# Kernel tuning notes

Hardware: AMD Instinct MI355X
Metric: run time of the kernel (lower is better)

Reference implementation:

```python
import jax, jax.numpy as jnp
import numpy as np

DT = 0.002   # solver step used for drive indexing
B = 2097152  # batched independent circuits (trailing axis of y)
T = 50000    # external drive time steps
NP = 59      # number of clamped scalar parameters


def setup_inputs() -> dict:
    key = jax.random.key(0)
    k1, k2, k3 = jax.random.split(key, 3)
    params = jax.random.uniform(k1, (NP,), jnp.float32, 0.5, 10.0)
    bounds_lo = jnp.full((NP,), 0.01, dtype=jnp.float32)
    bounds_hi = jnp.full((NP,), 100.0, dtype=jnp.float32)
    t = jnp.float32(12.345)
    y = jax.random.normal(k2, (12, B), jnp.float32) * 5.0
    external_drive = jax.random.normal(k3, (T, 6), jnp.float32)
    return {"params": params, "bounds_lo": bounds_lo, "bounds_hi": bounds_hi,
            "t": t, "y": y, "external_drive": external_drive}


def _S(v, e0, v0, r):
    # sigmoidal firing-rate function
    return 2.0 * e0 / (1.0 + jnp.exp(r * (v0 - v)))


def reference(params, bounds_lo, bounds_hi, t, y, external_drive):
    p = jnp.clip(params, bounds_lo, bounds_hi)
    (A_p23_p23, A_p23_p5, A_p23_st, A_p23_PV, A_p23_SST, A_p23_VIP, a_p23, e0_p23, v0_p23, r_p23,
     A_p5_p5, A_p5_st, A_p5_PV, A_p5_SST, a_p5, e0_p5, v0_p5, r_p5,
     A_st_p23, A_st_p5, A_st_st, A_st_PV, A_st_SST, a_st, e0_st, v0_st, r_st,
     B_PV_p23, B_PV_p5, B_PV_st, B_PV_PV, B_PV_SST, B_PV_VIP, b_PV, e0_PV, v0_PV, r_PV,
     B_SST_p23, B_SST_p5, B_SST_PV, B_SST_SST, B_SST_VIP, b_SST, e0_SST, v0_SST, r_SST,
     B_VIP_PV, B_VIP_SST, B_VIP_VIP, b_VIP, e0_VIP, v0_VIP, r_VIP,
     N_p23, N_p5, N_st, N_PV, N_SST, N_VIP) = p

    P23, P5, St, PV, SST, VIP, dP23, dP5, dSt, dPV, dSST, dVIP = y  # each [B]

    F_P23 = _S(P23, e0_p23, v0_p23, r_p23)
    F_P5  = _S(P5,  e0_p5,  v0_p5,  r_p5)
    F_St  = _S(St,  e0_st,  v0_st,  r_st)
    F_PV  = _S(PV,  e0_PV,  v0_PV,  r_PV)
    F_SST = _S(SST, e0_SST, v0_SST, r_SST)
    F_VIP = _S(VIP, e0_VIP, v0_VIP, r_VIP)

    n_t = external_drive.shape[0]
    t_idx = jnp.clip(t / DT, 0.0, n_t - 1).astype(jnp.int32)
    drive = jax.lax.dynamic_index_in_dim(external_drive, t_idx, axis=0, keepdims=False)  # [6]
    cc_p23, th_p5, th_st, th_PV, nm_SST, cc_VIP = drive[0], drive[1], drive[2], drive[3], drive[4], drive[5]

    dy6 = (cc_p23 + A_st_p23 * a_st * F_St * (N_st / N_p23)
           + A_p23_p23 * a_p23 * F_P23
           - B_PV_p23 * b_PV * F_PV * (N_PV / N_p23)
           - B_SST_p23 * b_SST * F_SST * (N_SST / N_p23)
           - 2.0 * a_p23 * dP23 - a_p23 ** 2 * P23)
    dy7 = (th_p5 + A_st_p5 * a_st * F_St * (N_st / N_p5)
           + A_p23_p5 * a_p23 * F_P23 * (N_p23 / N_p5)
           + A_p5_p5 * a_p5 * F_P5
           - B_PV_p5 * b_PV * F_PV * (N_PV / N_p5)
           - B_SST_p5 * b_SST * F_SST * (N_SST / N_p5)
           - 2.0 * a_p5 * dP5 - a_p5 ** 2 * P5)
    dy8 = (th_st + A_p23_st * a_p23 * F_P23 * (N_p23 / N_st)
           + A_p5_st * a_p5 * F_P5 * (N_p5 / N_st)
           - B_PV_st * b_PV * F_PV * (N_PV / N_st)
           - 2.0 * a_st * dSt - a_st ** 2 * St)
    dy9 = (th_PV + A_p23_PV * a_p23 * F_P23 * (N_p23 / N_PV)
           + A_p5_PV * a_p5 * F_P5 * (N_p5 / N_PV)
           + A_st_PV * a_st * F_St * (N_st / N_PV)
           - B_PV_PV * b_PV * F_PV
           - B_SST_PV * b_SST * F_SST * (N_SST / N_PV)
           - B_VIP_PV * b_VIP * F_VIP * (N_VIP / N_PV)
           - 2.0 * b_PV * dPV - b_PV ** 2 * PV)
    dy10 = (nm_SST + A_p23_SST * a_p23 * F_P23 * (N_p23 / N_SST)
            + A_p5_SST * a_p5 * F_P5 * (N_p5 / N_SST)
            + A_st_SST * a_st * F_St * (N_st / N_SST)
            - B_PV_SST * b_PV * F_PV * (N_PV / N_SST)
            - B_SST_SST * b_SST * F_SST
            - B_VIP_SST * b_VIP * F_VIP * (N_VIP / N_SST)
            - 2.0 * b_SST * dSST - b_SST ** 2 * SST)
    dy11 = (cc_VIP + A_p23_VIP * a_p23 * F_P23 * (N_p23 / N_VIP)
            - B_PV_VIP * b_PV * F_PV * (N_PV / N_VIP)
            - B_SST_VIP * b_SST * F_SST * (N_SST / N_VIP)
            - B_VIP_VIP * b_VIP * F_VIP
            - 2.0 * b_VIP * dVIP - b_VIP ** 2 * VIP)

    return jnp.stack([dP23, dP5, dSt, dPV, dSST, dVIP, dy6, dy7, dy8, dy9, dy10, dy11])
```

## Files before the change

kernel.cpp:

```cpp
#include <hip/hip_runtime.h>
#include <math.h>


__global__ __launch_bounds__(256) void cc_kernel(
    const float* __restrict__ params,
    const float* __restrict__ blo,
    const float* __restrict__ bhi,
    const float* __restrict__ tptr,
    const float* __restrict__ y,
    const float* __restrict__ drive,
    float* __restrict__ out,
    int n, int tsteps)
{
    __shared__ float sc[72];
    __shared__ float p[59];

    const int tid = threadIdx.x;
    if (tid < 59) {
        float v = params[tid];
        p[tid] = fminf(fmaxf(v, blo[tid]), bhi[tid]);
    }
    __syncthreads();

    if (tid == 0) {
        float A_p23_p23=p[0], A_p23_p5=p[1], A_p23_st=p[2], A_p23_PV=p[3],
              A_p23_SST=p[4], A_p23_VIP=p[5], a_p23=p[6], e0_p23=p[7],
              v0_p23=p[8], r_p23=p[9];
        float A_p5_p5=p[10], A_p5_st=p[11], A_p5_PV=p[12], A_p5_SST=p[13],
              a_p5=p[14], e0_p5=p[15], v0_p5=p[16], r_p5=p[17];
        float A_st_p23=p[18], A_st_p5=p[19], A_st_PV=p[21],
              A_st_SST=p[22], a_st=p[23], e0_st=p[24], v0_st=p[25], r_st=p[26];
        float B_PV_p23=p[27], B_PV_p5=p[28], B_PV_st=p[29], B_PV_PV=p[30],
              B_PV_SST=p[31], B_PV_VIP=p[32], b_PV=p[33], e0_PV=p[34],
              v0_PV=p[35], r_PV=p[36];
        float B_SST_p23=p[37], B_SST_p5=p[38], B_SST_PV=p[39], B_SST_SST=p[40],
              B_SST_VIP=p[41], b_SST=p[42], e0_SST=p[43], v0_SST=p[44], r_SST=p[45];
        float B_VIP_PV=p[46], B_VIP_SST=p[47], B_VIP_VIP=p[48], b_VIP=p[49],
              e0_VIP=p[50], v0_VIP=p[51], r_VIP=p[52];
        float N_p23=p[53], N_p5=p[54], N_st=p[55], N_PV=p[56], N_SST=p[57], N_VIP=p[58];

        const float rr[6] = {r_p23, r_p5, r_st, r_PV, r_SST, r_VIP};
        const float vv[6] = {v0_p23, v0_p5, v0_st, v0_PV, v0_SST, v0_VIP};
        const float ee[6] = {e0_p23, e0_p5, e0_st, e0_PV, e0_SST, e0_VIP};
        const float gg[6] = {a_p23, a_p5, a_st, b_PV, b_SST, b_VIP};
        for (int k = 0; k < 6; ++k) {
            sc[k]      = rr[k];
            sc[6 + k]  = rr[k] * vv[k];
            sc[12 + k] = 2.0f * ee[k];
            sc[18 + k] = 2.0f * gg[k];
            sc[24 + k] = gg[k] * gg[k];
        }

        float t = *tptr;
        float fi = fminf(fmaxf(t / 0.002f, 0.0f), (float)(tsteps - 1));
        int ti = (int)fi;
        for (int k = 0; k < 6; ++k) sc[30 + k] = drive[(size_t)ti * 6 + k];

        float M[36];
        for (int i = 0; i < 36; ++i) M[i] = 0.0f;
        M[0*6+0] =  A_p23_p23 * a_p23;
        M[0*6+2] =  A_st_p23  * a_st  * (N_st  / N_p23);
        M[0*6+3] = -B_PV_p23  * b_PV  * (N_PV  / N_p23);
        M[0*6+4] = -B_SST_p23 * b_SST * (N_SST / N_p23);

        M[1*6+0] =  A_p23_p5  * a_p23 * (N_p23 / N_p5);
        M[1*6+1] =  A_p5_p5   * a_p5;
        M[1*6+2] =  A_st_p5   * a_st  * (N_st  / N_p5);
        M[1*6+3] = -B_PV_p5   * b_PV  * (N_PV  / N_p5);
        M[1*6+4] = -B_SST_p5  * b_SST * (N_SST / N_p5);

        M[2*6+0] =  A_p23_st  * a_p23 * (N_p23 / N_st);
        M[2*6+1] =  A_p5_st   * a_p5  * (N_p5  / N_st);
        M[2*6+3] = -B_PV_st   * b_PV  * (N_PV  / N_st);

        M[3*6+0] =  A_p23_PV  * a_p23 * (N_p23 / N_PV);
        M[3*6+1] =  A_p5_PV   * a_p5  * (N_p5  / N_PV);
        M[3*6+2] =  A_st_PV   * a_st  * (N_st  / N_PV);
        M[3*6+3] = -B_PV_PV   * b_PV;
        M[3*6+4] = -B_SST_PV  * b_SST * (N_SST / N_PV);
        M[3*6+5] = -B_VIP_PV  * b_VIP * (N_VIP / N_PV);

        M[4*6+0] =  A_p23_SST * a_p23 * (N_p23 / N_SST);
        M[4*6+1] =  A_p5_SST  * a_p5  * (N_p5  / N_SST);
        M[4*6+2] =  A_st_SST  * a_st  * (N_st  / N_SST);
        M[4*6+3] = -B_PV_SST  * b_PV  * (N_PV  / N_SST);
        M[4*6+4] = -B_SST_SST * b_SST;
        M[4*6+5] = -B_VIP_SST * b_VIP * (N_VIP / N_SST);

        M[5*6+0] =  A_p23_VIP * a_p23 * (N_p23 / N_VIP);
        M[5*6+3] = -B_PV_VIP  * b_PV  * (N_PV  / N_VIP);
        M[5*6+4] = -B_SST_VIP * b_SST * (N_SST / N_VIP);
        M[5*6+5] = -B_VIP_VIP * b_VIP;

        for (int i = 0; i < 36; ++i) sc[36 + i] = M[i];
    }
    __syncthreads();

    const size_t i4 = ((size_t)blockIdx.x * blockDim.x + threadIdx.x) * 4;
    if (i4 + 3 >= (size_t)n && i4 >= (size_t)n) return;

    float4 v[12];
#pragma unroll
    for (int r = 0; r < 12; ++r)
        v[r] = *(const float4*)(y + (size_t)r * n + i4);

#pragma unroll
    for (int r = 0; r < 6; ++r)
        *(float4*)(out + (size_t)r * n + i4) = v[6 + r];

    float F[6][4];
#pragma unroll
    for (int k = 0; k < 6; ++k) {
        const float rk  = sc[k];
        const float rv0 = sc[6 + k];
        const float e2  = sc[12 + k];
        const float* vk = (const float*)&v[k];
#pragma unroll
        for (int j = 0; j < 4; ++j)
            F[k][j] = e2 / (1.0f + __expf(rv0 - rk * vk[j]));
    }

#pragma unroll
    for (int i = 0; i < 6; ++i) {
        const float dr  = sc[30 + i];
        const float tg  = sc[18 + i];
        const float gsq = sc[24 + i];
        const float* vi = (const float*)&v[i];
        const float* di = (const float*)&v[6 + i];
        float4 o;
        float* op = (float*)&o;
#pragma unroll
        for (int j = 0; j < 4; ++j) {
            float acc = dr;
#pragma unroll
            for (int k = 0; k < 6; ++k)
                acc = fmaf(sc[36 + i * 6 + k], F[k][j], acc);
            acc = fmaf(-tg, di[j], acc);
            acc = fmaf(-gsq, vi[j], acc);
            op[j] = acc;
        }
        *(float4*)(out + (size_t)(6 + i) * n + i4) = o;
    }
}

extern "C" void kernel_launch(void* const* d_in, const int* in_sizes, int n_in,
                              void* d_out, int out_size, void* d_ws, size_t ws_size,
                              hipStream_t stream) {
    const float* params = (const float*)d_in[0];
    const float* blo    = (const float*)d_in[1];
    const float* bhi    = (const float*)d_in[2];
    const float* tptr   = (const float*)d_in[3];
    const float* y      = (const float*)d_in[4];
    const float* drive  = (const float*)d_in[5];
    float* out = (float*)d_out;

    const int n      = in_sizes[4] / 12;
    const int tsteps = in_sizes[5] / 6;

    const int threads = 256;
    const int elems_per_block = threads * 4;
    const int blocks = (n + elems_per_block - 1) / elems_per_block;

    cc_kernel<<<blocks, threads, 0, stream>>>(params, blo, bhi, tptr, y, drive,
                                              out, n, tsteps);
}
```

Measured before the change: 37.77 us.

## Precompute coefficients in a setup kernel and use nontemporal output stores

Moves the per-block parameter clamping, coefficient and matrix construction into a separate one-block setup kernel that writes 72 coefficients to the workspace. The main kernel then only loads these into shared memory, which removes the serial single-thread setup that every block previously ran. Output stores become nontemporal to reduce cache pollution on the streaming write. The cost is an extra kernel launch and a global round trip for the coefficients.

```diff
diff --git a/kernel.cpp b/kernel.cpp
--- a/kernel.cpp
+++ b/kernel.cpp
@@ -2,111 +2,119 @@
 #include <math.h>
 
 
-__global__ __launch_bounds__(256) void cc_kernel(
+typedef float v4f __attribute__((ext_vector_type(4)));
+
+__global__ void setup_kernel(
     const float* __restrict__ params,
     const float* __restrict__ blo,
     const float* __restrict__ bhi,
     const float* __restrict__ tptr,
-    const float* __restrict__ y,
     const float* __restrict__ drive,
-    float* __restrict__ out,
-    int n, int tsteps)
+    float* __restrict__ sc_out,
+    int tsteps)
 {
-    __shared__ float sc[72];
     __shared__ float p[59];
-
     const int tid = threadIdx.x;
     if (tid < 59) {
         float v = params[tid];
         p[tid] = fminf(fmaxf(v, blo[tid]), bhi[tid]);
     }
     __syncthreads();
+    if (tid != 0) return;
 
-    if (tid == 0) {
-        float A_p23_p23=p[0], A_p23_p5=p[1], A_p23_st=p[2], A_p23_PV=p[3],
-              A_p23_SST=p[4], A_p23_VIP=p[5], a_p23=p[6], e0_p23=p[7],
-              v0_p23=p[8], r_p23=p[9];
-        float A_p5_p5=p[10], A_p5_st=p[11], A_p5_PV=p[12], A_p5_SST=p[13],
-              a_p5=p[14], e0_p5=p[15], v0_p5=p[16], r_p5=p[17];
-        float A_st_p23=p[18], A_st_p5=p[19], A_st_PV=p[21],
-              A_st_SST=p[22], a_st=p[23], e0_st=p[24], v0_st=p[25], r_st=p[26];
-        float B_PV_p23=p[27], B_PV_p5=p[28], B_PV_st=p[29], B_PV_PV=p[30],
-              B_PV_SST=p[31], B_PV_VIP=p[32], b_PV=p[33], e0_PV=p[34],
-              v0_PV=p[35], r_PV=p[36];
-        float B_SST_p23=p[37], B_SST_p5=p[38], B_SST_PV=p[39], B_SST_SST=p[40],
-              B_SST_VIP=p[41], b_SST=p[42], e0_SST=p[43], v0_SST=p[44], r_SST=p[45];
-        float B_VIP_PV=p[46], B_VIP_SST=p[47], B_VIP_VIP=p[48], b_VIP=p[49],
-              e0_VIP=p[50], v0_VIP=p[51], r_VIP=p[52];
-        float N_p23=p[53], N_p5=p[54], N_st=p[55], N_PV=p[56], N_SST=p[57], N_VIP=p[58];
+    float A_p23_p23=p[0], A_p23_p5=p[1], A_p23_st=p[2], A_p23_PV=p[3],
+          A_p23_SST=p[4], A_p23_VIP=p[5], a_p23=p[6], e0_p23=p[7],
+          v0_p23=p[8], r_p23=p[9];
+    float A_p5_p5=p[10], A_p5_st=p[11], A_p5_PV=p[12], A_p5_SST=p[13],
+          a_p5=p[14], e0_p5=p[15], v0_p5=p[16], r_p5=p[17];
+    float A_st_p23=p[18], A_st_p5=p[19], A_st_PV=p[21],
+          A_st_SST=p[22], a_st=p[23], e0_st=p[24], v0_st=p[25], r_st=p[26];
+    float B_PV_p23=p[27], B_PV_p5=p[28], B_PV_st=p[29], B_PV_PV=p[30],
+          B_PV_SST=p[31], B_PV_VIP=p[32], b_PV=p[33], e0_PV=p[34],
+          v0_PV=p[35], r_PV=p[36];
+    float B_SST_p23=p[37], B_SST_p5=p[38], B_SST_PV=p[39], B_SST_SST=p[40],
+          B_SST_VIP=p[41], b_SST=p[42], e0_SST=p[43], v0_SST=p[44], r_SST=p[45];
+    float B_VIP_PV=p[46], B_VIP_SST=p[47], B_VIP_VIP=p[48], b_VIP=p[49],
+          e0_VIP=p[50], v0_VIP=p[51], r_VIP=p[52];
+    float N_p23=p[53], N_p5=p[54], N_st=p[55], N_PV=p[56], N_SST=p[57], N_VIP=p[58];
 
-        const float rr[6] = {r_p23, r_p5, r_st, r_PV, r_SST, r_VIP};
-        const float vv[6] = {v0_p23, v0_p5, v0_st, v0_PV, v0_SST, v0_VIP};
-        const float ee[6] = {e0_p23, e0_p5, e0_st, e0_PV, e0_SST, e0_VIP};
-        const float gg[6] = {a_p23, a_p5, a_st, b_PV, b_SST, b_VIP};
-        for (int k = 0; k < 6; ++k) {
-            sc[k]      = rr[k];
-            sc[6 + k]  = rr[k] * vv[k];
-            sc[12 + k] = 2.0f * ee[k];
-            sc[18 + k] = 2.0f * gg[k];
-            sc[24 + k] = gg[k] * gg[k];
-        }
+    const float rr[6] = {r_p23, r_p5, r_st, r_PV, r_SST, r_VIP};
+    const float vv[6] = {v0_p23, v0_p5, v0_st, v0_PV, v0_SST, v0_VIP};
+    const float ee[6] = {e0_p23, e0_p5, e0_st, e0_PV, e0_SST, e0_VIP};
+    const float gg[6] = {a_p23, a_p5, a_st, b_PV, b_SST, b_VIP};
+    for (int k = 0; k < 6; ++k) {
+        sc_out[k]      = rr[k];
+        sc_out[6 + k]  = rr[k] * vv[k];
+        sc_out[12 + k] = 2.0f * ee[k];
+        sc_out[18 + k] = 2.0f * gg[k];
+        sc_out[24 + k] = gg[k] * gg[k];
+    }
 
-        float t = *tptr;
-        float fi = fminf(fmaxf(t / 0.002f, 0.0f), (float)(tsteps - 1));
-        int ti = (int)fi;
-        for (int k = 0; k < 6; ++k) sc[30 + k] = drive[(size_t)ti * 6 + k];
+    float t = *tptr;
+    float fi = fminf(fmaxf(t / 0.002f, 0.0f), (float)(tsteps - 1));
+    int ti = (int)fi;
+    for (int k = 0; k < 6; ++k) sc_out[30 + k] = drive[(size_t)ti * 6 + k];
 
-        float M[36];
-        for (int i = 0; i < 36; ++i) M[i] = 0.0f;
-        M[0*6+0] =  A_p23_p23 * a_p23;
-        M[0*6+2] =  A_st_p23  * a_st  * (N_st  / N_p23);
-        M[0*6+3] = -B_PV_p23  * b_PV  * (N_PV  / N_p23);
-        M[0*6+4] = -B_SST_p23 * b_SST * (N_SST / N_p23);
+    float M[36];
+    for (int i = 0; i < 36; ++i) M[i] = 0.0f;
+    M[0*6+0] =  A_p23_p23 * a_p23;
+    M[0*6+2] =  A_st_p23  * a_st  * (N_st  / N_p23);
+    M[0*6+3] = -B_PV_p23  * b_PV  * (N_PV  / N_p23);
+    M[0*6+4] = -B_SST_p23 * b_SST * (N_SST / N_p23);
 
-        M[1*6+0] =  A_p23_p5  * a_p23 * (N_p23 / N_p5);
-        M[1*6+1] =  A_p5_p5   * a_p5;
-        M[1*6+2] =  A_st_p5   * a_st  * (N_st  / N_p5);
-        M[1*6+3] = -B_PV_p5   * b_PV  * (N_PV  / N_p5);
-        M[1*6+4] = -B_SST_p5  * b_SST * (N_SST / N_p5);
+    M[1*6+0] =  A_p23_p5  * a_p23 * (N_p23 / N_p5);
+    M[1*6+1] =  A_p5_p5   * a_p5;
+    M[1*6+2] =  A_st_p5   * a_st  * (N_st  / N_p5);
+    M[1*6+3] = -B_PV_p5   * b_PV  * (N_PV  / N_p5);
+    M[1*6+4] = -B_SST_p5  * b_SST * (N_SST / N_p5);
 
-        M[2*6+0] =  A_p23_st  * a_p23 * (N_p23 / N_st);
-        M[2*6+1] =  A_p5_st   * a_p5  * (N_p5  / N_st);
-        M[2*6+3] = -B_PV_st   * b_PV  * (N_PV  / N_st);
+    M[2*6+0] =  A_p23_st  * a_p23 * (N_p23 / N_st);
+    M[2*6+1] =  A_p5_st   * a_p5  * (N_p5  / N_st);
+    M[2*6+3] = -B_PV_st   * b_PV  * (N_PV  / N_st);
 
-        M[3*6+0] =  A_p23_PV  * a_p23 * (N_p23 / N_PV);
-        M[3*6+1] =  A_p5_PV   * a_p5  * (N_p5  / N_PV);
-        M[3*6+2] =  A_st_PV   * a_st  * (N_st  / N_PV);
-        M[3*6+3] = -B_PV_PV   * b_PV;
-        M[3*6+4] = -B_SST_PV  * b_SST * (N_SST / N_PV);
-        M[3*6+5] = -B_VIP_PV  * b_VIP * (N_VIP / N_PV);
+    M[3*6+0] =  A_p23_PV  * a_p23 * (N_p23 / N_PV);
+    M[3*6+1] =  A_p5_PV   * a_p5  * (N_p5  / N_PV);
+    M[3*6+2] =  A_st_PV   * a_st  * (N_st  / N_PV);
+    M[3*6+3] = -B_PV_PV   * b_PV;
+    M[3*6+4] = -B_SST_PV  * b_SST * (N_SST / N_PV);
+    M[3*6+5] = -B_VIP_PV  * b_VIP * (N_VIP / N_PV);
 
-        M[4*6+0] =  A_p23_SST * a_p23 * (N_p23 / N_SST);
-        M[4*6+1] =  A_p5_SST  * a_p5  * (N_p5  / N_SST);
-        M[4*6+2] =  A_st_SST  * a_st  * (N_st  / N_SST);
-        M[4*6+3] = -B_PV_SST  * b_PV  * (N_PV  / N_SST);
-        M[4*6+4] = -B_SST_SST * b_SST;
-        M[4*6+5] = -B_VIP_SST * b_VIP * (N_VIP / N_SST);
+    M[4*6+0] =  A_p23_SST * a_p23 * (N_p23 / N_SST);
+    M[4*6+1] =  A_p5_SST  * a_p5  * (N_p5  / N_SST);
+    M[4*6+2] =  A_st_SST  * a_st  * (N_st  / N_SST);
+    M[4*6+3] = -B_PV_SST  * b_PV  * (N_PV  / N_SST);
+    M[4*6+4] = -B_SST_SST * b_SST;
+    M[4*6+5] = -B_VIP_SST * b_VIP * (N_VIP / N_SST);
 
-        M[5*6+0] =  A_p23_VIP * a_p23 * (N_p23 / N_VIP);
-        M[5*6+3] = -B_PV_VIP  * b_PV  * (N_PV  / N_VIP);
-        M[5*6+4] = -B_SST_VIP * b_SST * (N_SST / N_VIP);
-        M[5*6+5] = -B_VIP_VIP * b_VIP;
+    M[5*6+0] =  A_p23_VIP * a_p23 * (N_p23 / N_VIP);
+    M[5*6+3] = -B_PV_VIP  * b_PV  * (N_PV  / N_VIP);
+    M[5*6+4] = -B_SST_VIP * b_SST * (N_SST / N_VIP);
+    M[5*6+5] = -B_VIP_VIP * b_VIP;
 
-        for (int i = 0; i < 36; ++i) sc[36 + i] = M[i];
-    }
+    for (int i = 0; i < 36; ++i) sc_out[36 + i] = M[i];
+}
+
+__global__ __launch_bounds__(256) void cc_kernel(
+    const float* __restrict__ y,
+    const float* __restrict__ scg,
+    float* __restrict__ out,
+    int n)
+{
+    __shared__ float sc[72];
+    if (threadIdx.x < 72) sc[threadIdx.x] = scg[threadIdx.x];
     __syncthreads();
 
     const size_t i4 = ((size_t)blockIdx.x * blockDim.x + threadIdx.x) * 4;
-    if (i4 + 3 >= (size_t)n && i4 >= (size_t)n) return;
+    if (i4 >= (size_t)n) return;
 
-    float4 v[12];
+    v4f v[12];
 #pragma unroll
     for (int r = 0; r < 12; ++r)
-        v[r] = *(const float4*)(y + (size_t)r * n + i4);
+        v[r] = *(const v4f*)(y + (size_t)r * n + i4);
 
 #pragma unroll
     for (int r = 0; r < 6; ++r)
-        *(float4*)(out + (size_t)r * n + i4) = v[6 + r];
+        __builtin_nontemporal_store(v[6 + r], (v4f*)(out + (size_t)r * n + i4));
 
     float F[6][4];
 #pragma unroll
@@ -114,10 +122,9 @@
         const float rk  = sc[k];
         const float rv0 = sc[6 + k];
         const float e2  = sc[12 + k];
-        const float* vk = (const float*)&v[k];
 #pragma unroll
         for (int j = 0; j < 4; ++j)
-            F[k][j] = e2 / (1.0f + __expf(rv0 - rk * vk[j]));
+            F[k][j] = e2 / (1.0f + __expf(rv0 - rk * v[k][j]));
     }
 
 #pragma unroll
@@ -125,21 +132,18 @@
         const float dr  = sc[30 + i];
         const float tg  = sc[18 + i];
         const float gsq = sc[24 + i];
-        const float* vi = (const float*)&v[i];
-        const float* di = (const float*)&v[6 + i];
-        float4 o;
-        float* op = (float*)&o;
+        v4f o;
 #pragma unroll
         for (int j = 0; j < 4; ++j) {
             float acc = dr;
 #pragma unroll
             for (int k = 0; k < 6; ++k)
                 acc = fmaf(sc[36 + i * 6 + k], F[k][j], acc);
-            acc = fmaf(-tg, di[j], acc);
-            acc = fmaf(-gsq, vi[j], acc);
-            op[j] = acc;
+            acc = fmaf(-tg, v[6 + i][j], acc);
+            acc = fmaf(-gsq, v[i][j], acc);
+            o[j] = acc;
         }
-        *(float4*)(out + (size_t)(6 + i) * n + i4) = o;
+        __builtin_nontemporal_store(o, (v4f*)(out + (size_t)(6 + i) * n + i4));
     }
 }
 
@@ -153,14 +157,16 @@
     const float* y      = (const float*)d_in[4];
     const float* drive  = (const float*)d_in[5];
     float* out = (float*)d_out;
+    float* sc  = (float*)d_ws;
 
     const int n      = in_sizes[4] / 12;
     const int tsteps = in_sizes[5] / 6;
+
+    setup_kernel<<<1, 64, 0, stream>>>(params, blo, bhi, tptr, drive, sc, tsteps);
 
     const int threads = 256;
     const int elems_per_block = threads * 4;
     const int blocks = (n + elems_per_block - 1) / elems_per_block;
 
-    cc_kernel<<<blocks, threads, 0, stream>>>(params, blo, bhi, tptr, y, drive,
-                                              out, n, tsteps);
+    cc_kernel<<<blocks, threads, 0, stream>>>(y, sc, out, n);
 }
```

After: 42.37 us. 1.12x slower.
